# Performance work log

Measured on AMD Instinct MI355X. Metric: run time of the kernel, lower is better.

## Reference

```python
import jax, jax.numpy as jnp
import numpy as np

D_Z = 1024
D_MODEL = 4096
EPS = 1e-5  # torch LayerNorm default
CLAMP = 3.0


def setup_inputs() -> dict:
    key = jax.random.key(0)
    k_z, k_w, k_b = jax.random.split(key, 3)
    z = jax.random.normal(k_z, (8, 2048, D_Z), dtype=jnp.float32)
    # LayerNorm params (gamma=1, beta=0 init in torch; keep learnable form)
    ln_gamma = jnp.ones((D_Z,), dtype=jnp.float32)
    ln_beta = jnp.zeros((D_Z,), dtype=jnp.float32)
    # Linear: torch default init U(-1/sqrt(d_z), 1/sqrt(d_z))
    bound = 1.0 / np.sqrt(D_Z)
    W = jax.random.uniform(k_w, (D_Z, D_MODEL), minval=-bound, maxval=bound, dtype=jnp.float32)
    b = jax.random.uniform(k_b, (D_MODEL,), minval=-bound, maxval=bound, dtype=jnp.float32)
    scale = jnp.ones((1,), dtype=jnp.float32)
    return {"z": z, "ln_gamma": ln_gamma, "ln_beta": ln_beta, "W": W, "b": b, "scale": scale}


def reference(z, ln_gamma, ln_beta, W, b, scale):
    # LayerNorm over last dim
    mu = jnp.mean(z, axis=-1, keepdims=True)
    var = jnp.mean(jnp.square(z - mu), axis=-1, keepdims=True)
    zn = (z - mu) * jax.lax.rsqrt(var + EPS) * ln_gamma + ln_beta
    # Linear -> scalar scale -> tanh clamp
    x = (jnp.einsum('bsd,dm->bsm', zn, W) + b) * scale
    return jnp.tanh(x / CLAMP) * CLAMP
```

## Files before the change

kernel.cpp:

```cpp
#include <hip/hip_runtime.h>

#define M_DIM 16384
#define K_DIM 1024
#define N_DIM 4096
#define T_TILES (K_DIM / 32)

typedef __bf16 bf16x8 __attribute__((ext_vector_type(8)));
typedef float f32x16 __attribute__((ext_vector_type(16)));

__device__ __forceinline__ unsigned short f2bf(float f) {
    union { float f; unsigned int i; } v; v.f = f;
    unsigned int r = v.i + 0x7fffu + ((v.i >> 16) & 1u);
    return (unsigned short)(r >> 16);
}
__device__ __forceinline__ unsigned int pack2(float lo, float hi) {
    return ((unsigned int)f2bf(lo)) | (((unsigned int)f2bf(hi)) << 16);
}

__global__ __launch_bounds__(256) void prep_kernel(
        const float* __restrict__ z,
        const float* __restrict__ gamma,
        const float* __restrict__ beta,
        unsigned short* __restrict__ zn,
        const float* __restrict__ W,
        unsigned short* __restrict__ Wt) {
    __shared__ float t[32][33];
    const int tid = threadIdx.x;
    if (blockIdx.x < M_DIM / 4) {
        const int wave = tid >> 6;
        const int lane = tid & 63;
        const size_t row = (size_t)blockIdx.x * 4 + wave;
        const float* zr = z + row * K_DIM;

        float4 x[4];
#pragma unroll
        for (int v = 0; v < 4; v++) x[v] = *(const float4*)(zr + v * 256 + lane * 4);

        float s = 0.f, ss = 0.f;
#pragma unroll
        for (int v = 0; v < 4; v++) {
            s  += x[v].x + x[v].y + x[v].z + x[v].w;
            ss += x[v].x * x[v].x + x[v].y * x[v].y + x[v].z * x[v].z + x[v].w * x[v].w;
        }
#pragma unroll
        for (int o = 32; o; o >>= 1) { s += __shfl_xor(s, o, 64); ss += __shfl_xor(ss, o, 64); }
        const float mean = s * (1.f / K_DIM);
        const float var = ss * (1.f / K_DIM) - mean * mean;
        const float rstd = rsqrtf(var + 1e-5f);

#pragma unroll
        for (int v = 0; v < 4; v++) {
            float4 g = *(const float4*)(gamma + v * 256 + lane * 4);
            float4 b = *(const float4*)(beta + v * 256 + lane * 4);
            float o0 = (x[v].x - mean) * rstd * g.x + b.x;
            float o1 = (x[v].y - mean) * rstd * g.y + b.y;
            float o2 = (x[v].z - mean) * rstd * g.z + b.z;
            float o3 = (x[v].w - mean) * rstd * g.w + b.w;
            uint2 q; q.x = pack2(o0, o1); q.y = pack2(o2, o3);
            *(uint2*)(zn + row * K_DIM + v * 256 + lane * 4) = q;
        }
    } else {
        const int bid = blockIdx.x - M_DIM / 4;
        const int tx = tid & 31, ty = tid >> 5;
        const int n0 = (bid & (N_DIM / 32 - 1)) * 32, k0 = (bid / (N_DIM / 32)) * 32;
#pragma unroll
        for (int j = 0; j < 32; j += 8)
            t[ty + j][tx] = W[(size_t)(k0 + ty + j) * N_DIM + n0 + tx];
        __syncthreads();
#pragma unroll
        for (int j = 0; j < 32; j += 8)
            Wt[(size_t)(n0 + ty + j) * K_DIM + k0 + tx] = f2bf(t[tx][ty + j]);
    }
}

__device__ __forceinline__ void async_copy16(const unsigned short* g, unsigned short* l) {
    __builtin_amdgcn_global_load_lds(
        (const __attribute__((address_space(1))) unsigned int*)g,
        (__attribute__((address_space(3))) unsigned int*)l,
        16, 0, 0);
}

__global__ __launch_bounds__(512, 2) void gemm_kernel(
        const unsigned short* __restrict__ A,
        const unsigned short* __restrict__ B,
        const float* __restrict__ bias,
        const float* __restrict__ scale,
        float* __restrict__ out) {
    __shared__ __align__(16) unsigned short As[4][256 * 32];
    __shared__ __align__(16) unsigned short Bs[4][256 * 32];

    const int tid = threadIdx.x;
    const int wave = tid >> 6, lane = tid & 63;
    const int wm = wave >> 2, wn = wave & 3;
    const int l31 = lane & 31, lhi = lane >> 5;

    const int bid = blockIdx.y * gridDim.x + blockIdx.x;
    const int id2 = (bid & 7) * 128 + (bid >> 3);
    const int bm = id2 >> 4, bn = id2 & 15;

    const int r0 = tid >> 2;
    const int c0 = ((tid & 3) ^ ((tid >> 3) & 3)) << 3;
    const unsigned short* agA = A + (size_t)(bm * 256 + r0) * K_DIM + c0;
    const unsigned short* agB = B + (size_t)(bn * 256 + r0) * K_DIM + c0;
    const int ldsu = wave * 512;

#define STAGE_A(t_, s_) do { \
        const unsigned short* g_ = agA + (t_) * 32; \
        async_copy16(g_,                 &As[s_][ldsu]); \
        async_copy16(g_ + 128 * K_DIM,   &As[s_][4096 + ldsu]); } while (0)
#define STAGE_B(t_, s_) do { \
        const unsigned short* g_ = agB + (t_) * 32; \
        async_copy16(g_,                 &Bs[s_][ldsu]); \
        async_copy16(g_ + 128 * K_DIM,   &Bs[s_][4096 + ldsu]); } while (0)

    f32x16 acc[4][2] = {};
    const int swz = (l31 >> 1) & 3;
    bf16x8 a[2][2], b[2][2];

#define READ_A(s_, rb_) do { \
        const unsigned short* as_ = As[s_]; \
        _Pragma("unroll") \
        for (int i_ = 0; i_ < 2; ++i_) \
        _Pragma("unroll") \
        for (int ks_ = 0; ks_ < 2; ++ks_) \
            a[i_][ks_] = *(const bf16x8*)&as_[(wm * 128 + (rb_) + i_ * 32 + l31) * 32 + (((2 * ks_ + lhi) ^ swz) << 3)]; } while (0)
#define READ_B(s_) do { \
        const unsigned short* bs_ = Bs[s_]; \
        _Pragma("unroll") \
        for (int j_ = 0; j_ < 2; ++j_) \
        _Pragma("unroll") \
        for (int ks_ = 0; ks_ < 2; ++ks_) \
            b[j_][ks_] = *(const bf16x8*)&bs_[(wn * 64 + j_ * 32 + l31) * 32 + (((2 * ks_ + lhi) ^ swz) << 3)]; } while (0)

    STAGE_A(0, 0); STAGE_B(0, 0);
    STAGE_A(1, 1); STAGE_B(1, 1);
    STAGE_A(2, 2); STAGE_B(2, 2);
    asm volatile("s_waitcnt vmcnt(8)" ::: "memory");
    __builtin_amdgcn_s_barrier();
    asm volatile("" ::: "memory");
    READ_A(0, 0); READ_B(0);

#pragma unroll 4
    for (int t = 0; t < T_TILES; ++t) {
        const int s = t & 3, sn = (t + 1) & 3, ss = (t + 3) & 3;

        if (t + 3 < T_TILES) STAGE_A(t + 3, ss);
        asm volatile("" ::: "memory");
        __builtin_amdgcn_s_barrier();
        asm volatile("s_waitcnt lgkmcnt(0)" ::: "memory");
        __builtin_amdgcn_sched_barrier(0);
        __builtin_amdgcn_s_setprio(1);
#pragma unroll
        for (int ks = 0; ks < 2; ++ks)
#pragma unroll
            for (int i = 0; i < 2; ++i)
#pragma unroll
                for (int j = 0; j < 2; ++j)
                    acc[i][j] = __builtin_amdgcn_mfma_f32_32x32x16_bf16(a[i][ks], b[j][ks], acc[i][j], 0, 0, 0);
        __builtin_amdgcn_s_setprio(0);

        READ_A(s, 64);
        if (t + 3 < T_TILES) STAGE_B(t + 3, ss);
        asm volatile("" ::: "memory");
        __builtin_amdgcn_s_barrier();
        asm volatile("s_waitcnt lgkmcnt(0)" ::: "memory");
        __builtin_amdgcn_sched_barrier(0);
        __builtin_amdgcn_s_setprio(1);
#pragma unroll
        for (int ks = 0; ks < 2; ++ks)
#pragma unroll
            for (int i = 0; i < 2; ++i)
#pragma unroll
                for (int j = 0; j < 2; ++j)
                    acc[2 + i][j] = __builtin_amdgcn_mfma_f32_32x32x16_bf16(a[i][ks], b[j][ks], acc[2 + i][j], 0, 0, 0);
        __builtin_amdgcn_s_setprio(0);

        if (t < T_TILES - 1) {
            if (t < T_TILES - 3)       asm volatile("s_waitcnt vmcnt(8)" ::: "memory");
            else if (t == T_TILES - 3) asm volatile("s_waitcnt vmcnt(4)" ::: "memory");
            else                       asm volatile("s_waitcnt vmcnt(0)" ::: "memory");
            __builtin_amdgcn_s_barrier();
            asm volatile("" ::: "memory");
            READ_A(sn, 0); READ_B(sn);
        }
    }
#undef STAGE_A
#undef STAGE_B
#undef READ_A
#undef READ_B

    const float mfac = scale[0] * 0.96179669392236f;
#pragma unroll
    for (int j = 0; j < 2; ++j) {
        const int gcol = bn * 256 + wn * 64 + j * 32 + l31;
        const float bv = bias[gcol];
#pragma unroll
        for (int i = 0; i < 4; ++i) {
            const int rbase = bm * 256 + wm * 128 + i * 32 + 4 * lhi;
#pragma unroll
            for (int r = 0; r < 16; ++r) {
                const int grow = rbase + (r & 3) + 8 * (r >> 2);
                float tv = (acc[i][j][r] + bv) * mfac;
                float e = __builtin_amdgcn_exp2f(tv);
                out[(size_t)grow * N_DIM + gcol] = 3.f - 6.f * __builtin_amdgcn_rcpf(e + 1.f);
            }
        }
    }
}

extern "C" void kernel_launch(void* const* d_in, const int* in_sizes, int n_in,
                              void* d_out, int out_size, void* d_ws, size_t ws_size,
                              hipStream_t stream) {
    const float* z     = (const float*)d_in[0];
    const float* gamma = (const float*)d_in[1];
    const float* beta  = (const float*)d_in[2];
    const float* W     = (const float*)d_in[3];
    const float* b     = (const float*)d_in[4];
    const float* scale = (const float*)d_in[5];
    float* out = (float*)d_out;

    unsigned short* zn = (unsigned short*)d_ws;
    unsigned short* Wt = zn + (size_t)M_DIM * K_DIM;

    prep_kernel<<<M_DIM / 4 + (N_DIM / 32) * (K_DIM / 32), 256, 0, stream>>>(z, gamma, beta, zn, W, Wt);
    gemm_kernel<<<dim3(N_DIM / 256, M_DIM / 256), 512, 0, stream>>>(zn, Wt, b, scale, out);
}
```

Before: 464.1 us.

## Switch GEMM to BK=64 double-buffered LDS pipeline with 8-way swizzle

The K tile grows from 32 to 64, and the four-stage LDS ring of 32-wide tiles becomes a two-stage double buffer of 64-wide tiles, so the main loop runs half as many iterations and barriers. Each stage now loads A and B together with 8 async copies. The XOR swizzle widens to 8 chunks to match the 64-element rows. In exchange, prefetch depth drops to one tile ahead, register use rises from the larger fragment arrays, and the LDS read for the next tile is no longer overlapped with the previous MFMA block.

Result: no change. 463.2 us (-0.2%).

```diff
diff --git a/kernel.cpp b/kernel.cpp
--- a/kernel.cpp
+++ b/kernel.cpp
@@ -3,7 +3,7 @@
 #define M_DIM 16384
 #define K_DIM 1024
 #define N_DIM 4096
-#define T_TILES (K_DIM / 32)
+#define T_TILES (K_DIM / 64)
 
 typedef __bf16 bf16x8 __attribute__((ext_vector_type(8)));
 typedef float f32x16 __attribute__((ext_vector_type(16)));
@@ -86,8 +86,8 @@
         const float* __restrict__ bias,
         const float* __restrict__ scale,
         float* __restrict__ out) {
-    __shared__ __align__(16) unsigned short As[4][256 * 32];
-    __shared__ __align__(16) unsigned short Bs[4][256 * 32];
+    __shared__ __align__(16) unsigned short As[2][256 * 64];
+    __shared__ __align__(16) unsigned short Bs[2][256 * 64];
 
     const int tid = threadIdx.x;
     const int wave = tid >> 6, lane = tid & 63;
@@ -98,60 +98,60 @@
     const int id2 = (bid & 7) * 128 + (bid >> 3);
     const int bm = id2 >> 4, bn = id2 & 15;
 
-    const int r0 = tid >> 2;
-    const int c0 = ((tid & 3) ^ ((tid >> 3) & 3)) << 3;
+    const int r0 = tid >> 3;
+    const int c0 = ((tid & 7) ^ ((tid >> 3) & 7)) << 3;
     const unsigned short* agA = A + (size_t)(bm * 256 + r0) * K_DIM + c0;
     const unsigned short* agB = B + (size_t)(bn * 256 + r0) * K_DIM + c0;
     const int ldsu = wave * 512;
 
-#define STAGE_A(t_, s_) do { \
-        const unsigned short* g_ = agA + (t_) * 32; \
-        async_copy16(g_,                 &As[s_][ldsu]); \
-        async_copy16(g_ + 128 * K_DIM,   &As[s_][4096 + ldsu]); } while (0)
-#define STAGE_B(t_, s_) do { \
-        const unsigned short* g_ = agB + (t_) * 32; \
-        async_copy16(g_,                 &Bs[s_][ldsu]); \
-        async_copy16(g_ + 128 * K_DIM,   &Bs[s_][4096 + ldsu]); } while (0)
+#define STAGE(t_, s_) do { \
+        const unsigned short* gA_ = agA + (t_) * 64; \
+        const unsigned short* gB_ = agB + (t_) * 64; \
+        async_copy16(gA_,                 &As[s_][ldsu]); \
+        async_copy16(gA_ +  64 * K_DIM,   &As[s_][ldsu + 4096]); \
+        async_copy16(gA_ + 128 * K_DIM,   &As[s_][ldsu + 8192]); \
+        async_copy16(gA_ + 192 * K_DIM,   &As[s_][ldsu + 12288]); \
+        async_copy16(gB_,                 &Bs[s_][ldsu]); \
+        async_copy16(gB_ +  64 * K_DIM,   &Bs[s_][ldsu + 4096]); \
+        async_copy16(gB_ + 128 * K_DIM,   &Bs[s_][ldsu + 8192]); \
+        async_copy16(gB_ + 192 * K_DIM,   &Bs[s_][ldsu + 12288]); } while (0)
 
     f32x16 acc[4][2] = {};
-    const int swz = (l31 >> 1) & 3;
-    bf16x8 a[2][2], b[2][2];
-
-#define READ_A(s_, rb_) do { \
+    bf16x8 a[2][4], b[2][4];
+    const int rsw = l31 & 7;
+
+#define READ_A(s_, h_) do { \
         const unsigned short* as_ = As[s_]; \
         _Pragma("unroll") \
         for (int i_ = 0; i_ < 2; ++i_) \
         _Pragma("unroll") \
-        for (int ks_ = 0; ks_ < 2; ++ks_) \
-            a[i_][ks_] = *(const bf16x8*)&as_[(wm * 128 + (rb_) + i_ * 32 + l31) * 32 + (((2 * ks_ + lhi) ^ swz) << 3)]; } while (0)
+        for (int ks_ = 0; ks_ < 4; ++ks_) \
+            a[i_][ks_] = *(const bf16x8*)&as_[(wm * 128 + (h_) * 64 + i_ * 32 + l31) * 64 + (((2 * ks_ + lhi) ^ rsw) << 3)]; } while (0)
 #define READ_B(s_) do { \
         const unsigned short* bs_ = Bs[s_]; \
         _Pragma("unroll") \
         for (int j_ = 0; j_ < 2; ++j_) \
         _Pragma("unroll") \
-        for (int ks_ = 0; ks_ < 2; ++ks_) \
-            b[j_][ks_] = *(const bf16x8*)&bs_[(wn * 64 + j_ * 32 + l31) * 32 + (((2 * ks_ + lhi) ^ swz) << 3)]; } while (0)
-
-    STAGE_A(0, 0); STAGE_B(0, 0);
-    STAGE_A(1, 1); STAGE_B(1, 1);
-    STAGE_A(2, 2); STAGE_B(2, 2);
+        for (int ks_ = 0; ks_ < 4; ++ks_) \
+            b[j_][ks_] = *(const bf16x8*)&bs_[(wn * 64 + j_ * 32 + l31) * 64 + (((2 * ks_ + lhi) ^ rsw) << 3)]; } while (0)
+
+    STAGE(0, 0);
+    STAGE(1, 1);
     asm volatile("s_waitcnt vmcnt(8)" ::: "memory");
     __builtin_amdgcn_s_barrier();
     asm volatile("" ::: "memory");
-    READ_A(0, 0); READ_B(0);
-
-#pragma unroll 4
+
+#pragma unroll 2
     for (int t = 0; t < T_TILES; ++t) {
-        const int s = t & 3, sn = (t + 1) & 3, ss = (t + 3) & 3;
-
-        if (t + 3 < T_TILES) STAGE_A(t + 3, ss);
-        asm volatile("" ::: "memory");
-        __builtin_amdgcn_s_barrier();
+        const int s = t & 1;
+
+        READ_B(s);
+        READ_A(s, 0);
         asm volatile("s_waitcnt lgkmcnt(0)" ::: "memory");
         __builtin_amdgcn_sched_barrier(0);
         __builtin_amdgcn_s_setprio(1);
 #pragma unroll
-        for (int ks = 0; ks < 2; ++ks)
+        for (int ks = 0; ks < 4; ++ks)
 #pragma unroll
             for (int i = 0; i < 2; ++i)
 #pragma unroll
@@ -159,15 +159,12 @@
                     acc[i][j] = __builtin_amdgcn_mfma_f32_32x32x16_bf16(a[i][ks], b[j][ks], acc[i][j], 0, 0, 0);
         __builtin_amdgcn_s_setprio(0);
 
-        READ_A(s, 64);
-        if (t + 3 < T_TILES) STAGE_B(t + 3, ss);
-        asm volatile("" ::: "memory");
-        __builtin_amdgcn_s_barrier();
+        READ_A(s, 1);
         asm volatile("s_waitcnt lgkmcnt(0)" ::: "memory");
         __builtin_amdgcn_sched_barrier(0);
         __builtin_amdgcn_s_setprio(1);
 #pragma unroll
-        for (int ks = 0; ks < 2; ++ks)
+        for (int ks = 0; ks < 4; ++ks)
 #pragma unroll
             for (int i = 0; i < 2; ++i)
 #pragma unroll
@@ -176,16 +173,19 @@
         __builtin_amdgcn_s_setprio(0);
 
         if (t < T_TILES - 1) {
-            if (t < T_TILES - 3)       asm volatile("s_waitcnt vmcnt(8)" ::: "memory");
-            else if (t == T_TILES - 3) asm volatile("s_waitcnt vmcnt(4)" ::: "memory");
-            else                       asm volatile("s_waitcnt vmcnt(0)" ::: "memory");
             __builtin_amdgcn_s_barrier();
             asm volatile("" ::: "memory");
-            READ_A(sn, 0); READ_B(sn);
+            if (t + 2 < T_TILES) {
+                STAGE(t + 2, s);
+                asm volatile("s_waitcnt vmcnt(8)" ::: "memory");
+            } else {
+                asm volatile("s_waitcnt vmcnt(0)" ::: "memory");
+            }
+            __builtin_amdgcn_s_barrier();
+            asm volatile("" ::: "memory");
         }
     }
-#undef STAGE_A
-#undef STAGE_B
+#undef STAGE
 #undef READ_A
 #undef READ_B
 
```

## Switch GEMM inner loop from 32x32x16 to 16x16x32 bf16 MFMA tiles

Applied to the files above, without the earlier changes.

Replaces the 32x32x16 MFMA with 16x16x32 MFMA, regrouping the per-wave 128x64 tile into 8x4 16x16 accumulators with single-k-chunk fragment loads. LDS fragment reads move from software-prefetched at the end of the previous iteration to the start of each half-iteration, and an extra barrier is added between the two halves. This changes register usage and LDS access patterns. It also gives up the LDS-read/MFMA overlap the old prefetch provided and adds synchronisation.

Result: slower. 475.3 us (+2.4%).

```diff
diff --git a/kernel.cpp b/kernel.cpp
--- a/kernel.cpp
+++ b/kernel.cpp
@@ -6,7 +6,7 @@
 #define T_TILES (K_DIM / 32)
 
 typedef __bf16 bf16x8 __attribute__((ext_vector_type(8)));
-typedef float f32x16 __attribute__((ext_vector_type(16)));
+typedef float f32x4 __attribute__((ext_vector_type(4)));
 
 __device__ __forceinline__ unsigned short f2bf(float f) {
     union { float f; unsigned int i; } v; v.f = f;
@@ -92,7 +92,9 @@
     const int tid = threadIdx.x;
     const int wave = tid >> 6, lane = tid & 63;
     const int wm = wave >> 2, wn = wave & 3;
-    const int l31 = lane & 31, lhi = lane >> 5;
+    const int rl = lane & 15;
+    const int kc = lane >> 4;
+    const int swz = (rl >> 1) & 3;
 
     const int bid = blockIdx.y * gridDim.x + blockIdx.x;
     const int id2 = (bid & 7) * 128 + (bid >> 3);
@@ -113,24 +115,25 @@
         async_copy16(g_,                 &Bs[s_][ldsu]); \
         async_copy16(g_ + 128 * K_DIM,   &Bs[s_][4096 + ldsu]); } while (0)
 
-    f32x16 acc[4][2] = {};
-    const int swz = (l31 >> 1) & 3;
-    bf16x8 a[2][2], b[2][2];
-
-#define READ_A(s_, rb_) do { \
+    f32x4 acc[8][4] = {};
+    bf16x8 a[4], b[4];
+
+#define READ_A(s_, mh_) do { \
         const unsigned short* as_ = As[s_]; \
         _Pragma("unroll") \
-        for (int i_ = 0; i_ < 2; ++i_) \
-        _Pragma("unroll") \
-        for (int ks_ = 0; ks_ < 2; ++ks_) \
-            a[i_][ks_] = *(const bf16x8*)&as_[(wm * 128 + (rb_) + i_ * 32 + l31) * 32 + (((2 * ks_ + lhi) ^ swz) << 3)]; } while (0)
+        for (int mt_ = 0; mt_ < 4; ++mt_) \
+            a[mt_] = *(const bf16x8*)&as_[(wm * 128 + (mh_) * 64 + mt_ * 16 + rl) * 32 + ((kc ^ swz) << 3)]; } while (0)
 #define READ_B(s_) do { \
         const unsigned short* bs_ = Bs[s_]; \
         _Pragma("unroll") \
-        for (int j_ = 0; j_ < 2; ++j_) \
-        _Pragma("unroll") \
-        for (int ks_ = 0; ks_ < 2; ++ks_) \
-            b[j_][ks_] = *(const bf16x8*)&bs_[(wn * 64 + j_ * 32 + l31) * 32 + (((2 * ks_ + lhi) ^ swz) << 3)]; } while (0)
+        for (int nt_ = 0; nt_ < 4; ++nt_) \
+            b[nt_] = *(const bf16x8*)&bs_[(wn * 64 + nt_ * 16 + rl) * 32 + ((kc ^ swz) << 3)]; } while (0)
+#define MFG(mh_) do { \
+        _Pragma("unroll") \
+        for (int mt_ = 0; mt_ < 4; ++mt_) \
+        _Pragma("unroll") \
+        for (int nt_ = 0; nt_ < 4; ++nt_) \
+            acc[(mh_) * 4 + mt_][nt_] = __builtin_amdgcn_mfma_f32_16x16x32_bf16(a[mt_], b[nt_], acc[(mh_) * 4 + mt_][nt_], 0, 0, 0); } while (0)
 
     STAGE_A(0, 0); STAGE_B(0, 0);
     STAGE_A(1, 1); STAGE_B(1, 1);
@@ -138,69 +141,59 @@
     asm volatile("s_waitcnt vmcnt(8)" ::: "memory");
     __builtin_amdgcn_s_barrier();
     asm volatile("" ::: "memory");
-    READ_A(0, 0); READ_B(0);
 
 #pragma unroll 4
     for (int t = 0; t < T_TILES; ++t) {
-        const int s = t & 3, sn = (t + 1) & 3, ss = (t + 3) & 3;
-
+        const int s = t & 3, ss = (t + 3) & 3;
+
+        READ_A(s, 0); READ_B(s);
         if (t + 3 < T_TILES) STAGE_A(t + 3, ss);
         asm volatile("" ::: "memory");
         __builtin_amdgcn_s_barrier();
         asm volatile("s_waitcnt lgkmcnt(0)" ::: "memory");
         __builtin_amdgcn_sched_barrier(0);
         __builtin_amdgcn_s_setprio(1);
-#pragma unroll
-        for (int ks = 0; ks < 2; ++ks)
-#pragma unroll
-            for (int i = 0; i < 2; ++i)
-#pragma unroll
-                for (int j = 0; j < 2; ++j)
-                    acc[i][j] = __builtin_amdgcn_mfma_f32_32x32x16_bf16(a[i][ks], b[j][ks], acc[i][j], 0, 0, 0);
+        MFG(0);
         __builtin_amdgcn_s_setprio(0);
-
-        READ_A(s, 64);
+        asm volatile("" ::: "memory");
+        __builtin_amdgcn_s_barrier();
+        asm volatile("" ::: "memory");
+
+        READ_A(s, 1);
         if (t + 3 < T_TILES) STAGE_B(t + 3, ss);
         asm volatile("" ::: "memory");
         __builtin_amdgcn_s_barrier();
         asm volatile("s_waitcnt lgkmcnt(0)" ::: "memory");
         __builtin_amdgcn_sched_barrier(0);
         __builtin_amdgcn_s_setprio(1);
-#pragma unroll
-        for (int ks = 0; ks < 2; ++ks)
-#pragma unroll
-            for (int i = 0; i < 2; ++i)
-#pragma unroll
-                for (int j = 0; j < 2; ++j)
-                    acc[2 + i][j] = __builtin_amdgcn_mfma_f32_32x32x16_bf16(a[i][ks], b[j][ks], acc[2 + i][j], 0, 0, 0);
+        MFG(1);
         __builtin_amdgcn_s_setprio(0);
-
         if (t < T_TILES - 1) {
             if (t < T_TILES - 3)       asm volatile("s_waitcnt vmcnt(8)" ::: "memory");
             else if (t == T_TILES - 3) asm volatile("s_waitcnt vmcnt(4)" ::: "memory");
             else                       asm volatile("s_waitcnt vmcnt(0)" ::: "memory");
             __builtin_amdgcn_s_barrier();
             asm volatile("" ::: "memory");
-            READ_A(sn, 0); READ_B(sn);
         }
     }
 #undef STAGE_A
 #undef STAGE_B
 #undef READ_A
 #undef READ_B
+#undef MFG
 
     const float mfac = scale[0] * 0.96179669392236f;
 #pragma unroll
-    for (int j = 0; j < 2; ++j) {
-        const int gcol = bn * 256 + wn * 64 + j * 32 + l31;
+    for (int nt = 0; nt < 4; ++nt) {
+        const int gcol = bn * 256 + wn * 64 + nt * 16 + rl;
         const float bv = bias[gcol];
 #pragma unroll
-        for (int i = 0; i < 4; ++i) {
-            const int rbase = bm * 256 + wm * 128 + i * 32 + 4 * lhi;
-#pragma unroll
-            for (int r = 0; r < 16; ++r) {
-                const int grow = rbase + (r & 3) + 8 * (r >> 2);
-                float tv = (acc[i][j][r] + bv) * mfac;
+        for (int mt = 0; mt < 8; ++mt) {
+            const int rbase = bm * 256 + wm * 128 + mt * 16 + kc * 4;
+#pragma unroll
+            for (int r = 0; r < 4; ++r) {
+                const int grow = rbase + r;
+                float tv = (acc[mt][nt][r] + bv) * mfac;
                 float e = __builtin_amdgcn_exp2f(tv);
                 out[(size_t)grow * N_DIM + gcol] = 3.f - 6.f * __builtin_amdgcn_rcpf(e + 1.f);
             }
```
